# Performance work log

Hardware: AMD Instinct MI355X
Metric: run time of the kernel (lower is better)

The kernel has to match this reference:

```python
import jax, jax.numpy as jnp
import numpy as np

H = 2048          # hidden_size
NH = 16           # num query heads
NKV = 8           # num kv heads
HD = 128          # head_dim
T = 4096          # tokens (single causal prefill sequence)
THETA = 1000000.0
EPS = 1e-6
QS = NH * HD
KVS = NKV * HD
SCALE = HD ** -0.5


def setup_inputs() -> dict:
    key = jax.random.key(0)
    k0, k1, k2 = jax.random.split(key, 3)
    return {
        "positions": jnp.arange(T, dtype=jnp.int32),
        "hidden_states": jax.random.normal(k0, (T, H), jnp.float32),
        "w_qkv": jax.random.normal(k1, (H, QS + 2 * KVS), jnp.float32) * 0.02,
        "w_o": jax.random.normal(k2, (QS, H), jnp.float32) * 0.02,
        "q_norm_w": jnp.ones((HD,), jnp.float32),
        "k_norm_w": jnp.ones((HD,), jnp.float32),
    }


def _rmsnorm(x, w):
    # per-head RMSNorm over last dim (head_dim)
    return x * jax.lax.rsqrt(jnp.mean(x * x, axis=-1, keepdims=True) + EPS) * w


def _rope(x, cos, sin):
    # neox-style rotate-half RoPE; x: [T, nheads, HD], cos/sin: [T, 1, HD/2]
    x1, x2 = jnp.split(x, 2, axis=-1)
    return jnp.concatenate([x1 * cos - x2 * sin, x2 * cos + x1 * sin], axis=-1)


def reference(positions, hidden_states, w_qkv, w_o, q_norm_w, k_norm_w):
    # fused QKV projection then split
    qkv = hidden_states @ w_qkv                      # [T, QS+2*KVS]
    q, k, v = jnp.split(qkv, [QS, QS + KVS], axis=-1)
    q = _rmsnorm(q.reshape(T, NH, HD), q_norm_w)     # per-head QK RMSNorm
    k = _rmsnorm(k.reshape(T, NKV, HD), k_norm_w)
    v = v.reshape(T, NKV, HD)

    # RoPE over full head_dim
    inv_freq = 1.0 / (THETA ** (jnp.arange(0, HD, 2, dtype=jnp.float32) / HD))
    ang = positions.astype(jnp.float32)[:, None] * inv_freq  # [T, HD/2]
    cos = jnp.cos(ang)[:, None, :]
    sin = jnp.sin(ang)[:, None, :]
    q = _rope(q, cos, sin)
    k = _rope(k, cos, sin)

    # causal GQA attention (prefill path of RadixAttention)
    G = NH // NKV
    q4 = q.reshape(T, NKV, G, HD) * SCALE
    scores = jnp.einsum('tkgd,skd->kgts', q4, k)     # [NKV, G, T, T]
    causal = jnp.tril(jnp.ones((T, T), dtype=bool))
    scores = jnp.where(causal, scores, jnp.float32(-1e30))
    probs = jax.nn.softmax(scores, axis=-1)
    out = jnp.einsum('kgts,skd->tkgd', probs, v).reshape(T, QS)
    return out @ w_o
```

## Files before the change

kernel.cpp:

```cpp
#include <hip/hip_runtime.h>
#include <hip/hip_bf16.h>
#include <math.h>

#define T_TOK 4096
#define H_DIM 2048
#define NH 16
#define NKV 8
#define HD 128
#define QS (NH * HD)
#define KVS (NKV * HD)
#define QKV_W (QS + 2*KVS)
#define QSCALE (0.08838834764831845f * 1.4426950408889634f)
#define EPS 1e-6f

typedef short short8 __attribute__((ext_vector_type(8)));
typedef short short4v __attribute__((ext_vector_type(4)));
typedef float floatx4 __attribute__((ext_vector_type(4)));

#if __has_builtin(__builtin_amdgcn_exp2f)
#define EXP2(x) __builtin_amdgcn_exp2f(x)
#else
#define EXP2(x) exp2f(x)
#endif

__device__ __forceinline__ unsigned short f2bf(float f) {
    unsigned int u = __float_as_uint(f);
    unsigned int r = (u + 0x7FFFu + ((u >> 16) & 1u)) >> 16;
    return (unsigned short)r;
}
__device__ __forceinline__ float bf2f(unsigned short u) {
    unsigned int v = ((unsigned int)u) << 16;
    return __uint_as_float(v);
}
__device__ __forceinline__ unsigned int pk2(float a, float b) {
    union { __hip_bfloat162 h; unsigned int u; } c;
    c.h = __float22bfloat162_rn(make_float2(a, b));
    return c.u;
}

__device__ __forceinline__ void gload_lds16(const unsigned short* g, unsigned short* l) {
    __builtin_amdgcn_global_load_lds(
        (const __attribute__((address_space(1))) unsigned int*)(const void*)g,
        (__attribute__((address_space(3))) unsigned int*)(void*)l, 16, 0, 0);
}

__global__ __launch_bounds__(256) void cvt_bf16(const float* __restrict__ in,
                                                unsigned short* __restrict__ out) {
    int idx = (blockIdx.x * 256 + threadIdx.x) * 8;
    float4 v0 = *(const float4*)&in[idx];
    float4 v1 = *(const float4*)&in[idx + 4];
    short8 t;
    t[0] = (short)f2bf(v0.x); t[1] = (short)f2bf(v0.y);
    t[2] = (short)f2bf(v0.z); t[3] = (short)f2bf(v0.w);
    t[4] = (short)f2bf(v1.x); t[5] = (short)f2bf(v1.y);
    t[6] = (short)f2bf(v1.z); t[7] = (short)f2bf(v1.w);
    *(short8*)&out[idx] = t;
}

__global__ __launch_bounds__(256) void cvt_transpose(const float* __restrict__ in,
                                                     unsigned short* __restrict__ out,
                                                     int K, int N) {
    __shared__ __align__(16) unsigned short t[64][72];
    const int tid = threadIdx.x;
    const int n0 = blockIdx.x * 64, k0 = blockIdx.y * 64;
    const int r = tid >> 4, c4 = (tid & 15) * 4;
    #pragma unroll
    for (int i = 0; i < 4; ++i) {
        int kk = r + 16 * i;
        float4 v = *(const float4*)&in[(size_t)(k0 + kk) * N + n0 + c4];
        t[c4 + 0][kk] = f2bf(v.x); t[c4 + 1][kk] = f2bf(v.y);
        t[c4 + 2][kk] = f2bf(v.z); t[c4 + 3][kk] = f2bf(v.w);
    }
    __syncthreads();
    const int n = tid >> 2, c8 = (tid & 3) * 16;
    short8 a = *(const short8*)&t[n][c8];
    short8 b = *(const short8*)&t[n][c8 + 8];
    *(short8*)&out[(size_t)(n0 + n) * K + k0 + c8] = a;
    *(short8*)&out[(size_t)(n0 + n) * K + k0 + c8 + 8] = b;
}

template<bool C_BF16>
__global__ __launch_bounds__(512, 2) void gemm256(const unsigned short* __restrict__ A, int lda,
                                                  const unsigned short* __restrict__ Bt, int ldb,
                                                  void* __restrict__ Cptr, int ldc, int K, int nbx) {
    __shared__ __align__(16) unsigned short lds[4 * 16384];
    const int tid  = threadIdx.x;
    const int wave = tid >> 6, lane = tid & 63;
    const int quad = lane >> 4, l16 = lane & 15;
    const int wm = wave >> 2, wn = wave & 3;

    const int cpx = gridDim.x >> 3;
    const int swz = (blockIdx.x & 7) * cpx + (blockIdx.x >> 3);
    const int by = swz / nbx, bx = swz % nbx;
    const int bm = by * 256, bn = bx * 256;

    const int ch0 = wave * 64 + lane;
    const int ch1 = 512 + ch0;
    const int ar0 = ch0 >> 2, ac0 = ((ch0 & 3) ^ (ar0 & 3)) * 8;
    const int ar1 = ch1 >> 2, ac1 = ((ch1 & 3) ^ (ar1 & 3)) * 8;
    const unsigned short* a0 = A  + (size_t)(bm + ar0) * lda + ac0;
    const unsigned short* a1 = A  + (size_t)(bm + ar1) * lda + ac1;
    const unsigned short* b0 = Bt + (size_t)(bn + ar0) * ldb + ac0;
    const unsigned short* b1 = Bt + (size_t)(bn + ar1) * ldb + ac1;
    const unsigned du0 = (unsigned)(wave * 64) * 8;
    const unsigned du1 = (unsigned)(512 + wave * 64) * 8;

    auto stage = [&](int kofs, int sb) {
        gload_lds16(a0 + kofs, &lds[sb + du0]);
        gload_lds16(a1 + kofs, &lds[sb + du1]);
        gload_lds16(b0 + kofs, &lds[sb + 8192 + du0]);
        gload_lds16(b1 + kofs, &lds[sb + 8192 + du1]);
    };

    floatx4 acc[8][4] = {};
    const int arow = wm * 128 + l16;
    const int brow = wn * 64 + l16;
    const int sslot = (quad ^ (l16 & 3)) * 8;

    auto compute = [&](int cbo) {
        short8 bfr[4];
        #pragma unroll
        for (int ni = 0; ni < 4; ++ni)
            bfr[ni] = *(const short8*)&lds[cbo + 8192 + (brow + ni * 16) * 32 + sslot];
        __builtin_amdgcn_s_setprio(1);
        #pragma unroll
        for (int mi = 0; mi < 8; ++mi) {
            short8 afr = *(const short8*)&lds[cbo + (arow + mi * 16) * 32 + sslot];
            #pragma unroll
            for (int ni = 0; ni < 4; ++ni)
                acc[mi][ni] = __builtin_amdgcn_mfma_f32_16x16x32_bf16(afr, bfr[ni], acc[mi][ni], 0, 0, 0);
        }
        __builtin_amdgcn_s_setprio(0);
    };

    const int NT = K >> 5;
    stage(0,  0);
    stage(32, 16384);
    stage(64, 32768);

    int cb = 0;
    for (int t = 0; t < NT - 3; ++t) {
        stage((t + 3) * 32, (cb + 3 * 16384) & 65535);
        asm volatile("s_waitcnt vmcnt(12)" ::: "memory");
        __builtin_amdgcn_s_barrier();
        asm volatile("" ::: "memory");
        compute(cb);
        asm volatile("" ::: "memory");
        __builtin_amdgcn_s_barrier();
        cb = (cb + 16384) & 65535;
    }
    asm volatile("s_waitcnt vmcnt(8)" ::: "memory");
    __builtin_amdgcn_s_barrier();
    asm volatile("" ::: "memory");
    compute(cb);
    asm volatile("" ::: "memory");
    __builtin_amdgcn_s_barrier();
    cb = (cb + 16384) & 65535;

    asm volatile("s_waitcnt vmcnt(4)" ::: "memory");
    __builtin_amdgcn_s_barrier();
    asm volatile("" ::: "memory");
    compute(cb);
    asm volatile("" ::: "memory");
    __builtin_amdgcn_s_barrier();
    cb = (cb + 16384) & 65535;

    asm volatile("s_waitcnt vmcnt(0)" ::: "memory");
    __builtin_amdgcn_s_barrier();
    asm volatile("" ::: "memory");
    compute(cb);

    #pragma unroll
    for (int mi = 0; mi < 8; ++mi)
        #pragma unroll
        for (int ni = 0; ni < 4; ++ni)
            #pragma unroll
            for (int r = 0; r < 4; ++r) {
                int row = bm + wm * 128 + mi * 16 + quad * 4 + r;
                int col = bn + wn * 64 + ni * 16 + l16;
                if (C_BF16)
                    ((unsigned short*)Cptr)[(size_t)row * ldc + col] = f2bf(acc[mi][ni][r]);
                else
                    ((float*)Cptr)[(size_t)row * ldc + col] = acc[mi][ni][r];
            }
}

__global__ __launch_bounds__(256) void rms_rope_bf16(unsigned short* __restrict__ qkv,
                                                     const int* __restrict__ positions,
                                                     const float* __restrict__ qw,
                                                     const float* __restrict__ kw) {
    const int t = blockIdx.x;
    const int wave = threadIdx.x >> 6;
    const int lane = threadIdx.x & 63;
    const float pos = (float)positions[t];
    unsigned short* row = qkv + (size_t)t * QKV_W;
    const float inv_freq = powf(1000000.0f, -(float)lane / 64.0f);
    float sv, cv;
    sincosf(pos * inv_freq, &sv, &cv);
    for (int h = wave; h < NH + NKV; h += 4) {
        unsigned short* x = row + h * HD;
        const float* w = (h < NH) ? qw : kw;
        const float hs = (h < NH) ? QSCALE : 1.0f;
        float x1 = bf2f(x[lane]);
        float x2 = bf2f(x[lane + 64]);
        float ss = x1 * x1 + x2 * x2;
        #pragma unroll
        for (int off = 32; off > 0; off >>= 1) ss += __shfl_xor(ss, off, 64);
        float r = rsqrtf(ss * (1.0f / 128.0f) + EPS) * hs;
        float n1 = x1 * r * w[lane];
        float n2 = x2 * r * w[lane + 64];
        x[lane]      = f2bf(n1 * cv - n2 * sv);
        x[lane + 64] = f2bf(n2 * cv + n1 * sv);
    }
}

__global__ __launch_bounds__(256) void kv_pack(const unsigned short* __restrict__ qkv,
                                               unsigned short* __restrict__ Kp,
                                               unsigned short* __restrict__ Vp) {
    const int tile = blockIdx.x, kvh = blockIdx.y, tid = threadIdx.x;
    const int t0 = tile * 128;
    const size_t tb = (size_t)(kvh * 32 + tile) * 16384;
    #pragma unroll
    for (int i = 0; i < 8; ++i) {
        int cid = i * 256 + tid;
        int s = cid >> 4, c = cid & 15;
        short8 v = *(const short8*)&qkv[(size_t)(t0 + s) * QKV_W + QS + kvh * HD + c * 8];
        *(short8*)&Kp[tb + (s * 16 + (c ^ (s & 7))) * 8] = v;
    }
    __shared__ __align__(16) unsigned short Lt[128 * 136];
    #pragma unroll
    for (int i = 0; i < 8; ++i) {
        int cid = i * 256 + tid;
        int s = cid >> 4, c = cid & 15;
        short8 v = *(const short8*)&qkv[(size_t)(t0 + s) * QKV_W + QS + KVS + kvh * HD + c * 8];
        #pragma unroll
        for (int e = 0; e < 8; ++e)
            Lt[(c * 8 + e) * 136 + s] = (unsigned short)v[e];
    }
    __syncthreads();
    #pragma unroll
    for (int i = 0; i < 8; ++i) {
        int cid = i * 256 + tid;
        int d = cid >> 4, cs = cid & 15;
        short8 v = *(const short8*)&Lt[d * 136 + cs * 8];
        short8 w;
        if ((d >> 3) & 1) {
            #pragma unroll
            for (int e = 0; e < 8; ++e) w[e] = v[e ^ 4];
        } else w = v;
        *(short8*)&Vp[tb + (d * 16 + (cs ^ (d & 7))) * 8] = w;
    }
}

__global__ __launch_bounds__(256, 2) void attn_mfma(unsigned short* __restrict__ qkv,
                                                    const unsigned short* __restrict__ Kp,
                                                    const unsigned short* __restrict__ Vp) {
    __shared__ __align__(16) unsigned short Ks[128 * 128];
    __shared__ __align__(16) unsigned short Vs[128 * 128];
    const int bx = blockIdx.x;
    const int h = bx & 15, kvh = h >> 1;
    const int g = bx >> 4;
    const int qt = (g < 16) ? (31 - g) : (g - 16);
    const int tid = threadIdx.x;
    const int wave = tid >> 6, lane = tid & 63;
    const int quad = lane >> 4, l16 = lane & 15;
    const int t0 = qt * 128;
    const int wrow0 = t0 + wave * 32;
    const int swz = l16 & 7;
    const int hsel = (l16 >> 3) & 1;
    const int vhalf = ((quad & 1) ^ hsel) * 4;
    const int q2 = quad >> 1;

    short8 qf[2][4];
    #pragma unroll
    for (int rt = 0; rt < 2; ++rt)
        #pragma unroll
        for (int ks = 0; ks < 4; ++ks) {
            int rowg = t0 + wave * 32 + rt * 16 + l16;
            qf[rt][ks] = *(const short8*)&qkv[(size_t)rowg * QKV_W + h * HD + ks * 32 + quad * 8];
        }

    float l_s[2] = {};
    floatx4 oacc[2][8] = {};

    for (int st = 0; st <= qt; ++st) {
        const int s0 = st * 128;
        const unsigned short* kb = Kp + (size_t)(kvh * 32 + st) * 16384;
        const unsigned short* vb = Vp + (size_t)(kvh * 32 + st) * 16384;
        #pragma unroll
        for (int i = 0; i < 8; ++i) {
            int ch = i * 256 + tid;
            gload_lds16(kb + (size_t)ch * 8, Ks + (i * 256 + wave * 64) * 8);
        }
        #pragma unroll
        for (int i = 0; i < 8; ++i) {
            int ch = i * 256 + tid;
            gload_lds16(vb + (size_t)ch * 8, Vs + (i * 256 + wave * 64) * 8);
        }
        __syncthreads();

        const bool diag = (st == qt);
        #pragma unroll
        for (int ct = 0; ct < 8; ++ct) {
            const int smin = s0 + ct * 16;
            if (diag && smin > wrow0 + 31) continue;
            floatx4 sacc[2] = {};
            #pragma unroll
            for (int ks = 0; ks < 4; ++ks) {
                short8 kfr = *(const short8*)&Ks[(ct * 16 + l16) * 128 + ((ks * 4 + quad) ^ swz) * 8];
                sacc[0] = __builtin_amdgcn_mfma_f32_16x16x32_bf16(kfr, qf[0][ks], sacc[0], 0, 0, 0);
                sacc[1] = __builtin_amdgcn_mfma_f32_16x16x32_bf16(kfr, qf[1][ks], sacc[1], 0, 0, 0);
            }
            short4v pp[2];
            #pragma unroll
            for (int rt = 0; rt < 2; ++rt) {
                const int tg = wrow0 + rt * 16 + l16;
                float p[4];
                float lsum = 0.0f;
                #pragma unroll
                for (int r = 0; r < 4; ++r) {
                    float s = sacc[rt][r];
                    if (diag && (smin + quad * 4 + r > tg)) s = -1e30f;
                    p[r] = EXP2(s);
                    lsum += p[r];
                }
                l_s[rt] += lsum;
                union { short4v s4; unsigned int u[2]; } pk;
                pk.u[0] = pk2(p[0], p[1]);
                pk.u[1] = pk2(p[2], p[3]);
                pp[rt] = pk.s4;
            }
            const int vc = (((ct * 2 + q2) ^ swz)) * 8 + vhalf;
#if __has_builtin(__builtin_amdgcn_mfma_f32_16x16x16bf16_1k)
            #pragma unroll
            for (int dct = 0; dct < 8; ++dct) {
                short4v bfr = *(const short4v*)&Vs[(dct * 16 + l16) * 128 + vc];
                oacc[0][dct] = __builtin_amdgcn_mfma_f32_16x16x16bf16_1k(pp[0], bfr, oacc[0][dct], 0, 0, 0);
                oacc[1][dct] = __builtin_amdgcn_mfma_f32_16x16x16bf16_1k(pp[1], bfr, oacc[1][dct], 0, 0, 0);
            }
#else
            #pragma unroll
            for (int dct = 0; dct < 8; ++dct) {
                union { short8 s8; short4v s4[2]; } b;
                b.s4[0] = *(const short4v*)&Vs[(dct * 16 + l16) * 128 + vc];
                b.s4[1] = short4v{0, 0, 0, 0};
                #pragma unroll
                for (int rt = 0; rt < 2; ++rt) {
                    union { short8 s8; short4v s4[2]; } a;
                    a.s4[0] = pp[rt];
                    a.s4[1] = short4v{0, 0, 0, 0};
                    oacc[rt][dct] = __builtin_amdgcn_mfma_f32_16x16x32_bf16(a.s8, b.s8, oacc[rt][dct], 0, 0, 0);
                }
            }
#endif
        }
        __syncthreads();
    }

    float lred[2];
    #pragma unroll
    for (int rt = 0; rt < 2; ++rt) {
        float l = l_s[rt];
        l += __shfl_xor(l, 16, 64);
        l += __shfl_xor(l, 32, 64);
        lred[rt] = l;
    }
    #pragma unroll
    for (int rt = 0; rt < 2; ++rt)
        #pragma unroll
        for (int r = 0; r < 4; ++r) {
            float l = __shfl(lred[rt], quad * 4 + r, 64);
            float linv = 1.0f / l;
            int rowg = t0 + wave * 32 + rt * 16 + quad * 4 + r;
            #pragma unroll
            for (int dct = 0; dct < 8; ++dct)
                qkv[(size_t)rowg * QKV_W + h * HD + dct * 16 + l16] = f2bf(oacc[rt][dct][r] * linv);
        }
}

extern "C" void kernel_launch(void* const* d_in, const int* in_sizes, int n_in,
                              void* d_out, int out_size, void* d_ws, size_t ws_size,
                              hipStream_t stream) {
    const int*   positions = (const int*)d_in[0];
    const float* hidden    = (const float*)d_in[1];
    const float* w_qkv     = (const float*)d_in[2];
    const float* w_o       = (const float*)d_in[3];
    const float* q_norm_w  = (const float*)d_in[4];
    const float* k_norm_w  = (const float*)d_in[5];
    float* out = (float*)d_out;

    unsigned short* qkvb   = (unsigned short*)d_ws;
    unsigned short* h_bf   = (unsigned short*)((char*)d_ws + ((size_t)32 << 20));
    unsigned short* Kp     = (unsigned short*)((char*)d_ws + ((size_t)32 << 20));
    unsigned short* Vp     = (unsigned short*)((char*)d_ws + ((size_t)40 << 20));
    unsigned short* wqkv_t = (unsigned short*)((char*)d_ws + ((size_t)48 << 20));
    unsigned short* wo_t   = (unsigned short*)((char*)d_ws + ((size_t)48 << 20));

    cvt_bf16<<<(T_TOK * H_DIM) / (256 * 8), 256, 0, stream>>>(hidden, h_bf);
    cvt_transpose<<<dim3(QKV_W / 64, H_DIM / 64), 256, 0, stream>>>(w_qkv, wqkv_t, H_DIM, QKV_W);
    gemm256<true><<<dim3(256), 512, 0, stream>>>(
        h_bf, H_DIM, wqkv_t, H_DIM, qkvb, QKV_W, H_DIM, QKV_W / 256);
    rms_rope_bf16<<<T_TOK, 256, 0, stream>>>(qkvb, positions, q_norm_w, k_norm_w);
    kv_pack<<<dim3(T_TOK / 128, NKV), 256, 0, stream>>>(qkvb, Kp, Vp);
    cvt_transpose<<<dim3(H_DIM / 64, QS / 64), 256, 0, stream>>>(w_o, wo_t, QS, H_DIM);
    attn_mfma<<<512, 256, 0, stream>>>(qkvb, Kp, Vp);
    gemm256<false><<<dim3(128), 512, 0, stream>>>(
        qkvb, QKV_W, wo_t, QS, out, H_DIM, QS, H_DIM / 256);
}
```

Before: 384.5 us.

## Double-buffer attention K/V tiles at 64-key granularity with async prefetch

```diff
diff --git a/kernel.cpp b/kernel.cpp
--- a/kernel.cpp
+++ b/kernel.cpp
@@ -255,8 +255,8 @@
 __global__ __launch_bounds__(256, 2) void attn_mfma(unsigned short* __restrict__ qkv,
                                                     const unsigned short* __restrict__ Kp,
                                                     const unsigned short* __restrict__ Vp) {
-    __shared__ __align__(16) unsigned short Ks[128 * 128];
-    __shared__ __align__(16) unsigned short Vs[128 * 128];
+    __shared__ __align__(16) unsigned short Ks[2][64 * 128];
+    __shared__ __align__(16) unsigned short Vs[2][64 * 128];
     const int bx = blockIdx.x;
     const int h = bx & 15, kvh = h >> 1;
     const int g = bx >> 4;
@@ -283,34 +283,42 @@
     float l_s[2] = {};
     floatx4 oacc[2][8] = {};
 
-    for (int st = 0; st <= qt; ++st) {
-        const int s0 = st * 128;
-        const unsigned short* kb = Kp + (size_t)(kvh * 32 + st) * 16384;
-        const unsigned short* vb = Vp + (size_t)(kvh * 32 + st) * 16384;
-        #pragma unroll
-        for (int i = 0; i < 8; ++i) {
+    const unsigned short* kbase = Kp + (size_t)(kvh * 32) * 16384;
+    const unsigned short* vbase = Vp + (size_t)(kvh * 32) * 16384;
+
+    auto stage = [&](int st64, int b) {
+        const int h0 = st64 & 1;
+        const unsigned short* kb = kbase + (size_t)(st64 >> 1) * 16384 + h0 * 8192;
+        const unsigned short* vb = vbase + (size_t)(st64 >> 1) * 16384;
+        #pragma unroll
+        for (int i = 0; i < 4; ++i) {
             int ch = i * 256 + tid;
-            gload_lds16(kb + (size_t)ch * 8, Ks + (i * 256 + wave * 64) * 8);
-        }
-        #pragma unroll
-        for (int i = 0; i < 8; ++i) {
-            int ch = i * 256 + tid;
-            gload_lds16(vb + (size_t)ch * 8, Vs + (i * 256 + wave * 64) * 8);
-        }
-        __syncthreads();
-
-        const bool diag = (st == qt);
-        #pragma unroll
-        for (int ct = 0; ct < 8; ++ct) {
+            gload_lds16(kb + (size_t)ch * 8, &Ks[b][(i * 256 + wave * 64) * 8]);
+        }
+        #pragma unroll
+        for (int i = 0; i < 4; ++i) {
+            int idx = i * 256 + tid;
+            int d = idx >> 3, j = idx & 7;
+            gload_lds16(vb + (size_t)(d * 16 + h0 * 8 + j) * 8, &Vs[b][(i * 256 + wave * 64) * 8]);
+        }
+    };
+
+    auto compute = [&](int st64, int b) {
+        const int s0 = st64 * 64;
+        const bool diag = (st64 >= 2 * qt);
+        #pragma unroll
+        for (int ct = 0; ct < 4; ++ct) {
             const int smin = s0 + ct * 16;
             if (diag && smin > wrow0 + 31) continue;
             floatx4 sacc[2] = {};
+            __builtin_amdgcn_s_setprio(1);
             #pragma unroll
             for (int ks = 0; ks < 4; ++ks) {
-                short8 kfr = *(const short8*)&Ks[(ct * 16 + l16) * 128 + ((ks * 4 + quad) ^ swz) * 8];
+                short8 kfr = *(const short8*)&Ks[b][(ct * 16 + l16) * 128 + ((ks * 4 + quad) ^ swz) * 8];
                 sacc[0] = __builtin_amdgcn_mfma_f32_16x16x32_bf16(kfr, qf[0][ks], sacc[0], 0, 0, 0);
                 sacc[1] = __builtin_amdgcn_mfma_f32_16x16x32_bf16(kfr, qf[1][ks], sacc[1], 0, 0, 0);
             }
+            __builtin_amdgcn_s_setprio(0);
             short4v pp[2];
             #pragma unroll
             for (int rt = 0; rt < 2; ++rt) {
@@ -330,32 +338,51 @@
                 pk.u[1] = pk2(p[2], p[3]);
                 pp[rt] = pk.s4;
             }
-            const int vc = (((ct * 2 + q2) ^ swz)) * 8 + vhalf;
+            const int vc = ((ct * 2 + q2) ^ swz) * 8 + vhalf;
+            __builtin_amdgcn_s_setprio(1);
 #if __has_builtin(__builtin_amdgcn_mfma_f32_16x16x16bf16_1k)
             #pragma unroll
             for (int dct = 0; dct < 8; ++dct) {
-                short4v bfr = *(const short4v*)&Vs[(dct * 16 + l16) * 128 + vc];
+                short4v bfr = *(const short4v*)&Vs[b][(dct * 16 + l16) * 64 + vc];
                 oacc[0][dct] = __builtin_amdgcn_mfma_f32_16x16x16bf16_1k(pp[0], bfr, oacc[0][dct], 0, 0, 0);
                 oacc[1][dct] = __builtin_amdgcn_mfma_f32_16x16x16bf16_1k(pp[1], bfr, oacc[1][dct], 0, 0, 0);
             }
 #else
             #pragma unroll
             for (int dct = 0; dct < 8; ++dct) {
-                union { short8 s8; short4v s4[2]; } b;
-                b.s4[0] = *(const short4v*)&Vs[(dct * 16 + l16) * 128 + vc];
-                b.s4[1] = short4v{0, 0, 0, 0};
+                union { short8 s8; short4v s4[2]; } bb;
+                bb.s4[0] = *(const short4v*)&Vs[b][(dct * 16 + l16) * 64 + vc];
+                bb.s4[1] = short4v{0, 0, 0, 0};
                 #pragma unroll
                 for (int rt = 0; rt < 2; ++rt) {
                     union { short8 s8; short4v s4[2]; } a;
                     a.s4[0] = pp[rt];
                     a.s4[1] = short4v{0, 0, 0, 0};
-                    oacc[rt][dct] = __builtin_amdgcn_mfma_f32_16x16x32_bf16(a.s8, b.s8, oacc[rt][dct], 0, 0, 0);
+                    oacc[rt][dct] = __builtin_amdgcn_mfma_f32_16x16x32_bf16(a.s8, bb.s8, oacc[rt][dct], 0, 0, 0);
                 }
             }
 #endif
-        }
-        __syncthreads();
-    }
+            __builtin_amdgcn_s_setprio(0);
+        }
+    };
+
+    const int NT = 2 * (qt + 1);
+    int buf = 0;
+    stage(0, 0);
+    for (int t = 0; t < NT - 1; ++t) {
+        stage(t + 1, buf ^ 1);
+        asm volatile("s_waitcnt vmcnt(8)" ::: "memory");
+        __builtin_amdgcn_s_barrier();
+        asm volatile("" ::: "memory");
+        compute(t, buf);
+        asm volatile("" ::: "memory");
+        __builtin_amdgcn_s_barrier();
+        buf ^= 1;
+    }
+    asm volatile("s_waitcnt vmcnt(0)" ::: "memory");
+    __builtin_amdgcn_s_barrier();
+    asm volatile("" ::: "memory");
+    compute(NT - 1, buf);
 
     float lred[2];
     #pragma unroll
```

New measurement: 451.1 us. 17.3% more time.
